# Kernel optimization log

Hardware: AMD Instinct MI355X
Metric: run time of the kernel (lower is better)

Reference implementation:

```python
import jax, jax.numpy as jnp
import numpy as np

SCORE_THRESHOLD = 0.5
IOU_THRESHOLD = 0.5
N = 8192
IMG = 640.0


def setup_inputs() -> dict:
    key = jax.random.key(0)
    k1, k2, k3 = jax.random.split(key, 3)
    # valid xyxy boxes on a 640px canvas: x2 > x1, y2 > y1
    xy1 = jax.random.uniform(k1, (N, 2), dtype=jnp.float32) * (IMG - 64.0)
    wh = jax.random.uniform(k2, (N, 2), dtype=jnp.float32) * 96.0 + 4.0
    xyxy = jnp.concatenate([xy1, xy1 + wh], axis=1)  # [N,4]
    person_conf = jax.random.uniform(k3, (N,), dtype=jnp.float32)  # [N]
    return {"xyxy": xyxy, "person_conf": person_conf}


def _pairwise_iou(boxes):
    # boxes: [N,4] xyxy -> iou: [N,N]
    x1, y1, x2, y2 = boxes[:, 0], boxes[:, 1], boxes[:, 2], boxes[:, 3]
    area = (x2 - x1) * (y2 - y1)  # [N]
    ix1 = jnp.maximum(x1[:, None], x1[None, :])
    iy1 = jnp.maximum(y1[:, None], y1[None, :])
    ix2 = jnp.minimum(x2[:, None], x2[None, :])
    iy2 = jnp.minimum(y2[:, None], y2[None, :])
    iw = jnp.maximum(ix2 - ix1, 0.0)
    ih = jnp.maximum(iy2 - iy1, 0.0)
    inter = iw * ih
    union = area[:, None] + area[None, :] - inter
    return inter / jnp.maximum(union, 1e-9)


def reference(xyxy, person_conf):
    # score-threshold filter (as a mask to stay jit-compatible / fixed shape)
    valid = person_conf >= SCORE_THRESHOLD  # [N]
    # sort by score descending; invalid boxes sink to the bottom
    sort_scores = jnp.where(valid, person_conf, -jnp.inf)
    order = jnp.argsort(-sort_scores)  # [N]
    boxes_s = xyxy[order]              # [N,4]
    scores_s = person_conf[order]      # [N]
    valid_s = valid[order]             # [N]

    iou = _pairwise_iou(boxes_s)  # [N,N]
    idx = jnp.arange(N)

    def body(i, keep):
        # box i (if still kept) suppresses lower-scored overlapping boxes
        sup = keep[i] & (iou[i] > IOU_THRESHOLD) & (idx > i)
        return keep & ~sup

    keep = jax.lax.fori_loop(0, N, body, valid_s)  # [N] bool

    boxes_and_scores = jnp.concatenate([boxes_s, scores_s[:, None]], axis=1)  # [N,5]
    out = jnp.where(keep[:, None], boxes_and_scores, 0.0)  # suppressed rows zeroed
    return out, keep
```

## Files before the change

kernel.cpp:

```cpp
#include <hip/hip_runtime.h>

typedef unsigned long long u64;
typedef unsigned int u32;

static constexpr int N = 8192;
static constexpr int NW = N / 64;
static constexpr int CAPE = 12288;


__device__ __forceinline__ u64 make_key(float s, int i) {
  u32 adj = (s >= 0.5f) ? (__float_as_uint(s) + 1u) : 0u;
  return ((u64)adj << 32) | (u64)(u32)(N - 1 - i);
}

__global__ __launch_bounds__(1024)
void rank_scatter_kernel(const float4* __restrict__ xyxy, const float* __restrict__ conf,
                         float4* __restrict__ boxes_s, float* __restrict__ scores_s,
                         float* __restrict__ areas_s, int* __restrict__ ecount) {
  #pragma clang fp contract(off)
  __shared__ u64 sk[2048];
  __shared__ u32 cnt[64];
  const int tid = threadIdx.x;
  const int il = tid & 63;
  const int jq = tid >> 6;
  const int i = blockIdx.x * 64 + il;
  if (tid < 64) cnt[tid] = 0;
  if (blockIdx.x == 0 && tid == 0) *ecount = 0;
  const u64 ki = make_key(conf[i], i);
  u32 local = 0;
  for (int tile = 0; tile < 4; ++tile) {
    __syncthreads();
    int j0 = tile * 2048 + tid;
    sk[tid] = make_key(conf[j0], j0);
    int j1 = j0 + 1024;
    sk[1024 + tid] = make_key(conf[j1], j1);
    __syncthreads();
    const int base = jq * 128;
    #pragma unroll 8
    for (int k = 0; k < 128; ++k) local += (sk[base + k] > ki);
  }
  atomicAdd(&cnt[il], local);
  __syncthreads();
  if (tid < 64) {
    u32 r = cnt[tid];
    int ii = blockIdx.x * 64 + tid;
    float4 b = xyxy[ii];
    boxes_s[r] = b;
    scores_s[r] = conf[ii];
    areas_s[r] = (b.z - b.x) * (b.w - b.y);
  }
}

__global__ __launch_bounds__(1024)
void mask_kernel(const float4* __restrict__ boxes_s, const float* __restrict__ areas_s,
                 const float* __restrict__ scores_s,
                 u64* __restrict__ edgeW, u32* __restrict__ edgeM,
                 int* __restrict__ ecount) {
  #pragma clang fp contract(off)
  __shared__ float4 cb[16][64];
  __shared__ float  ca[16][64];
  const int tid = threadIdx.x;
  const int lane = tid & 63;
  const int wave = tid >> 6;
  const int yb = blockIdx.y;
  const double C = 0.5 + 0x1p-25;
  #pragma unroll
  for (int q = 0; q < 2; ++q) {
    const int xb = blockIdx.x * 32 + wave * 2 + q;
    if (xb < yb || scores_s[xb * 64] < 0.5f) continue;
    cb[wave][lane] = boxes_s[xb * 64 + lane];
    ca[wave][lane] = areas_s[xb * 64 + lane];
    const int i = yb * 64 + lane;
    const float4 rb = boxes_s[i];
    const float ra = areas_s[i];
    const float sc_i = scores_s[i];
    const int jbase = xb * 64;
    u64 w = 0;
    for (int p = 0; p < 64; ++p) {
      float4 c = cb[wave][p];
      float ix1 = fmaxf(rb.x, c.x);
      float iy1 = fmaxf(rb.y, c.y);
      float ix2 = fminf(rb.z, c.z);
      float iy2 = fminf(rb.w, c.w);
      float iw = fmaxf(ix2 - ix1, 0.0f);
      float ih = fmaxf(iy2 - iy1, 0.0f);
      float inter = iw * ih;
      float uni = fmaxf((ra + ca[wave][p]) - inter, 1e-9f);
      bool sup = ((double)inter > C * (double)uni);
      if (sup && (jbase + p > i)) w |= (1ull << p);
    }
    if (sc_i < 0.5f) w = 0;
    u64 nz = __ballot(w != 0ull);
    if (nz) {
      int base = 0;
      if (lane == 0) base = atomicAdd(ecount, __popcll(nz));
      base = __shfl(base, 0);
      if (w) {
        int idx = base + __popcll(nz & ((1ull << lane) - 1ull));
        if (idx < CAPE) {
          edgeW[idx] = w;
          edgeM[idx] = (u32)i | ((u32)xb << 16);
        }
      }
    }
  }
}

__global__ __launch_bounds__(256)
void fix_kernel(const u64* __restrict__ edgeWG, const u32* __restrict__ edgeMG,
                const int* __restrict__ ecount, const float* __restrict__ scores_s,
                u64* __restrict__ keepw) {
  __shared__ u64 ew[CAPE];
  __shared__ u32 em[CAPE];
  __shared__ u32 valid32[2 * NW];
  __shared__ u32 ext32[2 * NW];
  __shared__ u32 keep32[2 * NW];
  __shared__ u32 loc32[2][64];
  __shared__ u32 bcnt[8], boff[8];
  __shared__ int chg[2];
  const int tid = threadIdx.x;
  const int lane = tid & 63;

  if (tid < 8) bcnt[tid] = 0;
  if (tid < 256) ext32[tid] = 0;
  if (tid < 128) loc32[tid >> 6][tid & 63] = 0;
  for (int p = tid; p < N; p += 256) {
    u64 b = __ballot(scores_s[p] >= 0.5f);
    if (lane == 0) {
      valid32[(p >> 6) * 2]     = (u32)b;
      valid32[(p >> 6) * 2 + 1] = (u32)(b >> 32);
    }
  }
  int E = *ecount;
  if (E > CAPE) E = CAPE;
  __syncthreads();

  for (int e = tid; e < E; e += 256) {
    u32 m = edgeMG[e];
    int s = (m & 0xffff) >> 11, xs = (m >> 16) >> 5;
    atomicAdd(&bcnt[s * 2 + (xs != s)], 1u);
  }
  __syncthreads();
  if (tid == 0) {
    u32 acc = 0;
    #pragma unroll
    for (int b = 0; b < 8; ++b) { boff[b] = acc; acc += bcnt[b]; bcnt[b] = boff[b]; }
  }
  __syncthreads();
  for (int e = tid; e < E; e += 256) {
    u32 m = edgeMG[e];
    int s = (m & 0xffff) >> 11, xs = (m >> 16) >> 5;
    u32 idx = atomicAdd(&bcnt[s * 2 + (xs != s)], 1u);
    ew[idx] = edgeWG[e];
    em[idx] = m;
  }
  __syncthreads();

  for (int s = 0; s < 4; ++s) {
    if (tid < 64) {
      keep32[s * 64 + tid] = valid32[s * 64 + tid] & ~ext32[s * 64 + tid];
    }
    if (tid == 0) { chg[0] = 0; chg[1] = 0; }
    __syncthreads();
    const u32 l0 = boff[s * 2], l1 = boff[s * 2] + (bcnt[s * 2] - boff[s * 2]);
    const u32 lend = bcnt[s * 2];
    (void)l1;
    int par = 0;
    for (int it = 0; it < 4096; ++it) {
      for (u32 e = l0 + tid; e < lend; e += 256) {
        u32 m = em[e];
        int row = m & 0xffff;
        if ((keep32[row >> 5] >> (row & 31)) & 1u) {
          int x = m >> 16;
          u64 w = ew[e];
          atomicOr(&loc32[par][2 * (x & 31)],     (u32)w);
          atomicOr(&loc32[par][2 * (x & 31) + 1], (u32)(w >> 32));
        }
      }
      __syncthreads();
      if (tid < 64) {
        u32 nk = valid32[s * 64 + tid] & ~ext32[s * 64 + tid] & ~loc32[par][tid];
        if (nk != keep32[s * 64 + tid]) { keep32[s * 64 + tid] = nk; chg[par] = 1; }
        loc32[par ^ 1][tid] = 0;
      }
      if (tid == 64) chg[par ^ 1] = 0;
      __syncthreads();
      if (!chg[par]) break;
      par ^= 1;
    }
    const u32 x0 = boff[s * 2 + 1], xend = bcnt[s * 2 + 1];
    for (u32 e = x0 + tid; e < xend; e += 256) {
      u32 m = em[e];
      int row = m & 0xffff;
      if ((keep32[row >> 5] >> (row & 31)) & 1u) {
        int x = m >> 16;
        u64 w = ew[e];
        atomicOr(&ext32[2 * x],     (u32)w);
        atomicOr(&ext32[2 * x + 1], (u32)(w >> 32));
      }
    }
    if (tid < 128) loc32[tid >> 6][tid & 63] = 0;
    __syncthreads();
  }
  if (tid < 128)
    keepw[tid] = ((u64)keep32[2 * tid + 1] << 32) | (u64)keep32[2 * tid];
}

__global__ __launch_bounds__(256)
void write_kernel(const float4* __restrict__ boxes_s, const float* __restrict__ scores_s,
                  const u64* __restrict__ keepw, float* __restrict__ out) {
  const int s = blockIdx.x * 256 + threadIdx.x;
  bool keep = (keepw[s >> 6] >> (s & 63)) & 1ull;
  float4 b = boxes_s[s];
  float sc = scores_s[s];
  float* row = out + (u64)s * 5;
  if (keep) {
    row[0] = b.x; row[1] = b.y; row[2] = b.z; row[3] = b.w; row[4] = sc;
    out[N * 5 + s] = 1.0f;
  } else {
    row[0] = 0.0f; row[1] = 0.0f; row[2] = 0.0f; row[3] = 0.0f; row[4] = 0.0f;
    out[N * 5 + s] = 0.0f;
  }
}

extern "C" void kernel_launch(void* const* d_in, const int* in_sizes, int n_in,
                              void* d_out, int out_size, void* d_ws, size_t ws_size,
                              hipStream_t stream) {
  const float4* xyxy = (const float4*)d_in[0];
  const float* conf  = (const float*)d_in[1];
  char* ws = (char*)d_ws;
  float4* boxes_s   = (float4*)(ws + 0);
  float*  scores_s  = (float*)(ws + 131072);
  float*  areas_s   = (float*)(ws + 163840);
  int*    ecount    = (int*)(ws + 196608);
  u64*    keepw     = (u64*)(ws + 196616);
  u64*    edgeW     = (u64*)(ws + 197696);
  u32*    edgeM     = (u32*)(ws + 296000);
  float*  out       = (float*)d_out;

  rank_scatter_kernel<<<N / 64, 1024, 0, stream>>>(xyxy, conf, boxes_s,
                                                   scores_s, areas_s, ecount);
  dim3 mg(4, NW);
  mask_kernel<<<mg, 1024, 0, stream>>>(boxes_s, areas_s, scores_s,
                                       edgeW, edgeM, ecount);
  fix_kernel<<<1, 256, 0, stream>>>(edgeW, edgeM, ecount, scores_s, keepw);
  write_kernel<<<N / 256, 256, 0, stream>>>(boxes_s, scores_s, keepw, out);
}
```

Baseline: 129.2 us.

## Fuse write into single-block fix kernel and drop edge bucket sort

Merges the output write into the single-block fix kernel, which removes one launch and the keepw round-trip through global memory. Drops the counting-sort bucketing of edges. Instead every fixed-point iteration scans all edges with fully unrolled predicated loops and filters by segment. The iteration cap drops from 4096 to 256. This saves the sort passes and a launch, but each iteration now scans the whole edge list, and the 8192-row write runs on only 256 threads.

Measured after the change: 151.1 us. 1.17x slower.

```diff
diff --git a/kernel.cpp b/kernel.cpp
--- a/kernel.cpp
+++ b/kernel.cpp
@@ -107,74 +107,60 @@
 }
 
 __global__ __launch_bounds__(256)
-void fix_kernel(const u64* __restrict__ edgeWG, const u32* __restrict__ edgeMG,
-                const int* __restrict__ ecount, const float* __restrict__ scores_s,
-                u64* __restrict__ keepw) {
-  __shared__ u64 ew[CAPE];
-  __shared__ u32 em[CAPE];
+void fix_write_kernel(const u64* __restrict__ edgeWG, const u32* __restrict__ edgeMG,
+                      const int* __restrict__ ecount, const float* __restrict__ scores_s,
+                      const float4* __restrict__ boxes_s, float* __restrict__ out) {
+  __shared__ u64 ewl[CAPE];
+  __shared__ u32 eml[CAPE];
   __shared__ u32 valid32[2 * NW];
   __shared__ u32 ext32[2 * NW];
   __shared__ u32 keep32[2 * NW];
   __shared__ u32 loc32[2][64];
-  __shared__ u32 bcnt[8], boff[8];
   __shared__ int chg[2];
   const int tid = threadIdx.x;
   const int lane = tid & 63;
 
-  if (tid < 8) bcnt[tid] = 0;
-  if (tid < 256) ext32[tid] = 0;
-  if (tid < 128) loc32[tid >> 6][tid & 63] = 0;
-  for (int p = tid; p < N; p += 256) {
+  int E = *ecount;
+  if (E > CAPE) E = CAPE;
+
+  #pragma unroll
+  for (int k = 0; k < CAPE / 256; ++k) {
+    int e = tid + k * 256;
+    if (e < E) { ewl[e] = edgeWG[e]; eml[e] = edgeMG[e]; }
+  }
+  #pragma unroll
+  for (int k = 0; k < N / 256; ++k) {
+    int p = tid + k * 256;
     u64 b = __ballot(scores_s[p] >= 0.5f);
     if (lane == 0) {
       valid32[(p >> 6) * 2]     = (u32)b;
       valid32[(p >> 6) * 2 + 1] = (u32)(b >> 32);
     }
   }
-  int E = *ecount;
-  if (E > CAPE) E = CAPE;
+  if (tid < 256) ext32[tid] = 0;
+  if (tid < 128) loc32[tid >> 6][tid & 63] = 0;
   __syncthreads();
 
-  for (int e = tid; e < E; e += 256) {
-    u32 m = edgeMG[e];
-    int s = (m & 0xffff) >> 11, xs = (m >> 16) >> 5;
-    atomicAdd(&bcnt[s * 2 + (xs != s)], 1u);
-  }
-  __syncthreads();
-  if (tid == 0) {
-    u32 acc = 0;
-    #pragma unroll
-    for (int b = 0; b < 8; ++b) { boff[b] = acc; acc += bcnt[b]; bcnt[b] = boff[b]; }
-  }
-  __syncthreads();
-  for (int e = tid; e < E; e += 256) {
-    u32 m = edgeMG[e];
-    int s = (m & 0xffff) >> 11, xs = (m >> 16) >> 5;
-    u32 idx = atomicAdd(&bcnt[s * 2 + (xs != s)], 1u);
-    ew[idx] = edgeWG[e];
-    em[idx] = m;
-  }
-  __syncthreads();
-
   for (int s = 0; s < 4; ++s) {
-    if (tid < 64) {
+    if (tid < 64)
       keep32[s * 64 + tid] = valid32[s * 64 + tid] & ~ext32[s * 64 + tid];
-    }
     if (tid == 0) { chg[0] = 0; chg[1] = 0; }
     __syncthreads();
-    const u32 l0 = boff[s * 2], l1 = boff[s * 2] + (bcnt[s * 2] - boff[s * 2]);
-    const u32 lend = bcnt[s * 2];
-    (void)l1;
     int par = 0;
-    for (int it = 0; it < 4096; ++it) {
-      for (u32 e = l0 + tid; e < lend; e += 256) {
-        u32 m = em[e];
-        int row = m & 0xffff;
-        if ((keep32[row >> 5] >> (row & 31)) & 1u) {
+    for (int it = 0; it < 256; ++it) {
+      #pragma unroll
+      for (int k = 0; k < CAPE / 256; ++k) {
+        int e = tid + k * 256;
+        if (e < E) {
+          u32 m = eml[e];
+          int row = m & 0xffff;
           int x = m >> 16;
-          u64 w = ew[e];
-          atomicOr(&loc32[par][2 * (x & 31)],     (u32)w);
-          atomicOr(&loc32[par][2 * (x & 31) + 1], (u32)(w >> 32));
+          if ((row >> 11) == s && (x >> 5) == s &&
+              ((keep32[row >> 5] >> (row & 31)) & 1u)) {
+            u64 w = ewl[e];
+            atomicOr(&loc32[par][2 * (x & 31)],     (u32)w);
+            atomicOr(&loc32[par][2 * (x & 31) + 1], (u32)(w >> 32));
+          }
         }
       }
       __syncthreads();
@@ -188,38 +174,37 @@
       if (!chg[par]) break;
       par ^= 1;
     }
-    const u32 x0 = boff[s * 2 + 1], xend = bcnt[s * 2 + 1];
-    for (u32 e = x0 + tid; e < xend; e += 256) {
-      u32 m = em[e];
-      int row = m & 0xffff;
-      if ((keep32[row >> 5] >> (row & 31)) & 1u) {
+    #pragma unroll
+    for (int k = 0; k < CAPE / 256; ++k) {
+      int e = tid + k * 256;
+      if (e < E) {
+        u32 m = eml[e];
+        int row = m & 0xffff;
         int x = m >> 16;
-        u64 w = ew[e];
-        atomicOr(&ext32[2 * x],     (u32)w);
-        atomicOr(&ext32[2 * x + 1], (u32)(w >> 32));
+        if ((row >> 11) == s && (x >> 5) != s &&
+            ((keep32[row >> 5] >> (row & 31)) & 1u)) {
+          u64 w = ewl[e];
+          atomicOr(&ext32[2 * x],     (u32)w);
+          atomicOr(&ext32[2 * x + 1], (u32)(w >> 32));
+        }
       }
     }
     if (tid < 128) loc32[tid >> 6][tid & 63] = 0;
     __syncthreads();
   }
-  if (tid < 128)
-    keepw[tid] = ((u64)keep32[2 * tid + 1] << 32) | (u64)keep32[2 * tid];
-}
-
-__global__ __launch_bounds__(256)
-void write_kernel(const float4* __restrict__ boxes_s, const float* __restrict__ scores_s,
-                  const u64* __restrict__ keepw, float* __restrict__ out) {
-  const int s = blockIdx.x * 256 + threadIdx.x;
-  bool keep = (keepw[s >> 6] >> (s & 63)) & 1ull;
-  float4 b = boxes_s[s];
-  float sc = scores_s[s];
-  float* row = out + (u64)s * 5;
-  if (keep) {
-    row[0] = b.x; row[1] = b.y; row[2] = b.z; row[3] = b.w; row[4] = sc;
-    out[N * 5 + s] = 1.0f;
-  } else {
-    row[0] = 0.0f; row[1] = 0.0f; row[2] = 0.0f; row[3] = 0.0f; row[4] = 0.0f;
-    out[N * 5 + s] = 0.0f;
+
+  for (int r = tid; r < N; r += 256) {
+    bool keep = (keep32[r >> 5] >> (r & 31)) & 1u;
+    float4 b = boxes_s[r];
+    float sc = scores_s[r];
+    float* row = out + (u64)r * 5;
+    if (keep) {
+      row[0] = b.x; row[1] = b.y; row[2] = b.z; row[3] = b.w; row[4] = sc;
+      out[N * 5 + r] = 1.0f;
+    } else {
+      row[0] = 0.0f; row[1] = 0.0f; row[2] = 0.0f; row[3] = 0.0f; row[4] = 0.0f;
+      out[N * 5 + r] = 0.0f;
+    }
   }
 }
 
@@ -233,7 +218,6 @@
   float*  scores_s  = (float*)(ws + 131072);
   float*  areas_s   = (float*)(ws + 163840);
   int*    ecount    = (int*)(ws + 196608);
-  u64*    keepw     = (u64*)(ws + 196616);
   u64*    edgeW     = (u64*)(ws + 197696);
   u32*    edgeM     = (u32*)(ws + 296000);
   float*  out       = (float*)d_out;
@@ -243,6 +227,6 @@
   dim3 mg(4, NW);
   mask_kernel<<<mg, 1024, 0, stream>>>(boxes_s, areas_s, scores_s,
                                        edgeW, edgeM, ecount);
-  fix_kernel<<<1, 256, 0, stream>>>(edgeW, edgeM, ecount, scores_s, keepw);
-  write_kernel<<<N / 256, 256, 0, stream>>>(boxes_s, scores_s, keepw, out);
-}
+  fix_write_kernel<<<1, 256, 0, stream>>>(edgeW, edgeM, ecount,
+                                          scores_s, boxes_s, out);
+}
```
